# Optimization experiments

Hardware: AMD Instinct MI355X
Metric: run time of the kernel (lower is better)

## Reference

```python
import jax, jax.numpy as jnp
import numpy as np

NUM_GRAPHS = 512


def setup_inputs() -> dict:
    key = jax.random.key(0)
    ks = jax.random.split(key, 8)
    N, E, D, H = 50000, 800000, 128, 128
    x = jax.random.normal(ks[0], (N, D), dtype=jnp.float32)
    edge_attr = jax.random.normal(ks[1], (E, 8), dtype=jnp.float32)
    s = 1.0 / np.sqrt(D)
    W1 = jax.random.normal(ks[2], (D, H), dtype=jnp.float32) * s
    W2 = jax.random.normal(ks[3], (H, H), dtype=jnp.float32) * s
    W3 = jax.random.normal(ks[4], (H, H), dtype=jnp.float32) * s
    b1 = jnp.zeros((H,), jnp.float32)
    b2 = jnp.zeros((H,), jnp.float32)
    b3 = jnp.zeros((H,), jnp.float32)
    edge_index = jax.random.randint(ks[5], (2, E), 0, N, dtype=jnp.int64)
    batch = jnp.sort(jax.random.randint(ks[6], (N,), 0, NUM_GRAPHS, dtype=jnp.int64))
    return {"x": x, "edge_attr": edge_attr, "W1": W1, "b1": b1, "W2": W2,
            "b2": b2, "W3": W3, "b3": b3, "edge_index": edge_index, "batch": batch}


def reference(x, edge_attr, W1, b1, W2, b2, W3, b3, edge_index, batch):
    # edge_attr is accepted but unused (GCNConv ignores it), matching the source.
    N = x.shape[0]
    src, dst = edge_index[0], edge_index[1]
    loop = jnp.arange(N, dtype=src.dtype)
    src_f = jnp.concatenate([src, loop])  # self-loops appended (PyG GCNConv default)
    dst_f = jnp.concatenate([dst, loop])
    # symmetric degree normalization on A + I (deg >= 1 thanks to self-loops)
    deg = jax.ops.segment_sum(jnp.ones(src_f.shape[0], x.dtype), dst_f, num_segments=N)
    dinv = deg ** -0.5
    coef = (dinv[src_f] * dinv[dst_f])[:, None]  # [E+N, 1]

    def gcn_conv(h, W, b):
        h = h @ W                                   # linear first (PyG order)
        agg = jax.ops.segment_sum(h[src_f] * coef, dst_f, num_segments=N)
        return agg + b

    h = jax.nn.relu(gcn_conv(x, W1, b1))   # dropout is identity at inference
    h = jax.nn.relu(gcn_conv(h, W2, b2))
    h = jax.nn.relu(gcn_conv(h, W3, b3))

    # global_mean_pool over graph ids
    sums = jax.ops.segment_sum(h, batch, num_segments=NUM_GRAPHS)
    cnts = jax.ops.segment_sum(jnp.ones((N,), h.dtype), batch, num_segments=NUM_GRAPHS)
    return sums / jnp.maximum(cnts, 1.0)[:, None]
```

## Files before the change

kernel.cpp:

```cpp
#include <hip/hip_runtime.h>
#include <hip/hip_bf16.h>


#define TPB 256
#define CSTRIDE 16
typedef unsigned short u16;
typedef unsigned int u32;
typedef __attribute__((ext_vector_type(8))) __bf16 bf16x8;
typedef __attribute__((ext_vector_type(8))) u16 u16x8;
typedef __attribute__((ext_vector_type(4))) float f32x4;

__device__ __forceinline__ u16 f2b(float f) {
    __bf16 b = (__bf16)f;
    return __builtin_bit_cast(u16, b);
}
__device__ __forceinline__ float b2f_lo(u32 w) { return __builtin_bit_cast(float, w << 16); }
__device__ __forceinline__ float b2f_hi(u32 w) { return __builtin_bit_cast(float, w & 0xffff0000u); }

__device__ __forceinline__ bf16x8 cvt8(float4 u0, float4 u1) {
    u16x8 r;
    r[0] = f2b(u0.x); r[1] = f2b(u0.y); r[2] = f2b(u0.z); r[3] = f2b(u0.w);
    r[4] = f2b(u1.x); r[5] = f2b(u1.y); r[6] = f2b(u1.z); r[7] = f2b(u1.w);
    return __builtin_bit_cast(bf16x8, r);
}

__device__ __forceinline__ void countslot_body(int bid, const int* __restrict__ dst,
                                               int* cnt, u16* __restrict__ aux, int E) {
    int e = (bid * TPB + (int)threadIdx.x) * 4;
    if (e + 3 < E) {
        int4 d = *(const int4*)(dst + e);
        ushort4 a;
        a.x = (u16)atomicAdd(&cnt[d.x * CSTRIDE], 1);
        a.y = (u16)atomicAdd(&cnt[d.y * CSTRIDE], 1);
        a.z = (u16)atomicAdd(&cnt[d.z * CSTRIDE], 1);
        a.w = (u16)atomicAdd(&cnt[d.w * CSTRIDE], 1);
        *(ushort4*)(aux + e) = a;
    } else {
        for (; e < E; ++e) aux[e] = (u16)atomicAdd(&cnt[dst[e] * CSTRIDE], 1);
    }
}

__global__ __launch_bounds__(TPB) void k_scan1(const int* __restrict__ cnt, int* rowptr,
                                               int* bsum, int N) {
    __shared__ int tmp[TPB];
    int t = threadIdx.x;
    int i = blockIdx.x * TPB + t;
    int v = (i < N) ? cnt[(size_t)i * CSTRIDE] : 0;
    tmp[t] = v;
    __syncthreads();
    for (int off = 1; off < TPB; off <<= 1) {
        int y = (t >= off) ? tmp[t - off] : 0;
        __syncthreads();
        tmp[t] += y;
        __syncthreads();
    }
    if (i < N) rowptr[i] = tmp[t] - v;
    if (t == TPB - 1) bsum[blockIdx.x] = tmp[t];
}

__global__ __launch_bounds__(TPB) void k_scan3(int* rowptr, const int* __restrict__ bsum,
                                               const int* __restrict__ cnt, float* dinv,
                                               int N, int total, int nb) {
    __shared__ int tmp[TPB];
    int t = threadIdx.x;
    tmp[t] = (t < nb) ? bsum[t] : 0;
    __syncthreads();
    for (int off = 1; off < TPB; off <<= 1) {
        int y = (t >= off) ? tmp[t - off] : 0;
        __syncthreads();
        tmp[t] += y;
        __syncthreads();
    }
    int pre = (blockIdx.x == 0) ? 0 : tmp[blockIdx.x - 1];
    int i = blockIdx.x * TPB + t;
    if (i < N) {
        rowptr[i] += pre;
        dinv[i] = 1.0f / sqrtf((float)(cnt[(size_t)i * CSTRIDE] + 1));
    }
    if (i == 0) rowptr[N] = total;
}

__global__ __launch_bounds__(TPB) void k_fill_scale(const int* __restrict__ src,
                                                    const int* __restrict__ dst,
                                                    const int* __restrict__ rowptr,
                                                    const u16* __restrict__ aux,
                                                    u16* __restrict__ cols, int E, int nbF,
                                                    u16* __restrict__ g,
                                                    const float* __restrict__ dinv, int N) {
    int b = blockIdx.x;
    if (b < nbF) {
        int e = (b * TPB + (int)threadIdx.x) * 4;
        if (e + 3 < E) {
            int4 s = *(const int4*)(src + e);
            int4 d = *(const int4*)(dst + e);
            ushort4 a = *(const ushort4*)(aux + e);
            cols[rowptr[d.x] + a.x] = (u16)s.x;
            cols[rowptr[d.y] + a.y] = (u16)s.y;
            cols[rowptr[d.z] + a.z] = (u16)s.z;
            cols[rowptr[d.w] + a.w] = (u16)s.w;
        } else {
            for (; e < E; ++e) cols[rowptr[dst[e]] + aux[e]] = (u16)src[e];
        }
    } else {
        int e8 = (b - nbF) * TPB + (int)threadIdx.x;
        if (e8 < N * 16) {
            int row = e8 >> 4;
            int off = (e8 & 15) * 8;
            float dv = dinv[row];
            u16* p = g + (size_t)row * 128 + off;
            uint4 v = *(uint4*)p;
            uint4 o;
            o.x = (u32)f2b(dv * b2f_lo(v.x)) | ((u32)f2b(dv * b2f_hi(v.x)) << 16);
            o.y = (u32)f2b(dv * b2f_lo(v.y)) | ((u32)f2b(dv * b2f_hi(v.y)) << 16);
            o.z = (u32)f2b(dv * b2f_lo(v.z)) | ((u32)f2b(dv * b2f_hi(v.z)) << 16);
            o.w = (u32)f2b(dv * b2f_lo(v.w)) | ((u32)f2b(dv * b2f_hi(v.w)) << 16);
            *(uint4*)p = o;
        }
    }
}

__device__ __forceinline__ void prepw_body(int bb, const float* __restrict__ Wa,
                                           const float* __restrict__ Wb,
                                           const float* __restrict__ Wc,
                                           u16* __restrict__ Wta, u16* __restrict__ Wtb,
                                           u16* __restrict__ Wtc) {
    int m = bb >> 3;
    const float* W = m == 0 ? Wa : (m == 1 ? Wb : Wc);
    u16* Wt = m == 0 ? Wta : (m == 1 ? Wtb : Wtc);
    int t = (bb & 7) * TPB + (int)threadIdx.x;
    int n = t >> 4, c = t & 15;
    u16x8 r;
#pragma unroll
    for (int j = 0; j < 8; ++j) r[j] = f2b(W[(8 * c + j) * 128 + n]);
    int cs = c ^ (n & 15);
    *(u16x8*)(Wt + n * 128 + cs * 8) = r;
}

__global__ __launch_bounds__(TPB) void k_zero_prep(int* cnt, int N, int nbZ4,
                                                   const float* __restrict__ Wa,
                                                   const float* __restrict__ Wb,
                                                   const float* __restrict__ Wc,
                                                   u16* __restrict__ Wta,
                                                   u16* __restrict__ Wtb,
                                                   u16* __restrict__ Wtc,
                                                   u16* __restrict__ bufA,
                                                   u16* __restrict__ bufB) {
    int b = blockIdx.x;
    if (b < nbZ4) {
        int i = b * TPB + (int)threadIdx.x;
        if (i < N * (CSTRIDE / 4)) ((int4*)cnt)[i] = (int4){0, 0, 0, 0};
    } else if (b < nbZ4 + 24) {
        prepw_body(b - nbZ4, Wa, Wb, Wc, Wta, Wtb, Wtc);
    } else {
        int t = threadIdx.x;
        uint4 z = (uint4){0, 0, 0, 0};
        if (t < 16) *(uint4*)(bufA + (size_t)N * 128 + t * 8) = z;
        else if (t < 32) *(uint4*)(bufB + (size_t)N * 128 + (t - 16) * 8) = z;
    }
}

template <bool F32IN, bool SCALE>
__device__ __forceinline__ void gemm_body(int bid, const void* __restrict__ Ain,
                                          const u16* __restrict__ Wt,
                                          u16* __restrict__ C, int N,
                                          const float* __restrict__ dinv) {
    __shared__ u16 Ws[128 * 128];
    int t = threadIdx.x;
    {
        const uint4* s = (const uint4*)Wt;
        uint4* d = (uint4*)Ws;
#pragma unroll
        for (int i = 0; i < 8; ++i) d[t + 256 * i] = s[t + 256 * i];
    }
    __syncthreads();
    int wave = t >> 6, lane = t & 63;
    int li = lane & 15, lq = lane >> 4;
    int r0 = bid * 128 + wave * 32;
    f32x4 acc[2][8];
#pragma unroll
    for (int i = 0; i < 2; ++i)
#pragma unroll
        for (int f = 0; f < 8; ++f) acc[i][f] = (f32x4){0.f, 0.f, 0.f, 0.f};

    int ra = r0 + li, rb = ra + 16;
    size_t ra_c = (size_t)(ra < N ? ra : N - 1);
    size_t rb_c = (size_t)(rb < N ? rb : N - 1);
#pragma unroll
    for (int kc = 0; kc < 4; ++kc) {
        int koff = 32 * kc + 8 * lq;
        bf16x8 a0, a1;
        if constexpr (F32IN) {
            const float* A = (const float*)Ain;
            const float4* p0 = (const float4*)(A + ra_c * 128 + koff);
            const float4* p1 = (const float4*)(A + rb_c * 128 + koff);
            a0 = cvt8(p0[0], p0[1]);
            a1 = cvt8(p1[0], p1[1]);
        } else {
            const u16* A = (const u16*)Ain;
            a0 = *(const bf16x8*)(A + ra_c * 128 + koff);
            a1 = *(const bf16x8*)(A + rb_c * 128 + koff);
        }
#pragma unroll
        for (int f = 0; f < 8; ++f) {
            int n = 16 * f + li;
            int chunk = (4 * kc + lq) ^ li;
            bf16x8 b = *(const bf16x8*)(Ws + n * 128 + chunk * 8);
            acc[0][f] = __builtin_amdgcn_mfma_f32_16x16x32_bf16(a0, b, acc[0][f], 0, 0, 0);
            acc[1][f] = __builtin_amdgcn_mfma_f32_16x16x32_bf16(a1, b, acc[1][f], 0, 0, 0);
        }
    }
#pragma unroll
    for (int ri = 0; ri < 2; ++ri)
#pragma unroll
        for (int r = 0; r < 4; ++r) {
            int row = r0 + 16 * ri + 4 * lq + r;
            if (row < N) {
                float dv = 1.0f;
                if constexpr (SCALE) dv = dinv[row];
#pragma unroll
                for (int f = 0; f < 8; ++f)
                    C[(size_t)row * 128 + 16 * f + li] = f2b(dv * acc[ri][f][r]);
            }
        }
}

template <bool F32IN, bool SCALE>
__global__ __launch_bounds__(TPB) void k_gemm(const void* __restrict__ Ain,
                                              const u16* __restrict__ Wt,
                                              u16* __restrict__ C, int N,
                                              const float* __restrict__ dinv) {
    gemm_body<F32IN, SCALE>(blockIdx.x, Ain, Wt, C, N, dinv);
}

__global__ __launch_bounds__(TPB) void k_gemm1_count(const void* __restrict__ x,
                                                     const u16* __restrict__ Wt1,
                                                     u16* __restrict__ C, int N, int nbG,
                                                     const int* __restrict__ dst,
                                                     int* cnt, u16* __restrict__ aux, int E) {
    int b = blockIdx.x;
    if (b < nbG) {
        gemm_body<true, false>(b, x, Wt1, C, N, nullptr);
    } else {
        countslot_body(b - nbG, dst, cnt, aux, E);
    }
}

#define AGG_ISS(BUF, T)                                                    \
    {                                                                      \
        _Pragma("unroll") for (int u = 0; u < 8; ++u) {                    \
            int col = __shfl(cg[T], u, 8);                                 \
            const u16* p = g + (size_t)col * 128 + fo;                     \
            asm volatile("global_load_dwordx4 %0, %1, off sc0"             \
                         : "=v"(BUF[u]) : "v"(p));                         \
        }                                                                  \
    }
#define AGG_CONS(BUF)                                                      \
    {                                                                      \
        _Pragma("unroll") for (int u = 0; u < 8; ++u) {                    \
            a[0] += b2f_lo(BUF[u].x); a[1] += b2f_hi(BUF[u].x);            \
            a[2] += b2f_lo(BUF[u].y); a[3] += b2f_hi(BUF[u].y);            \
            a[4] += b2f_lo(BUF[u].z); a[5] += b2f_hi(BUF[u].z);            \
            a[6] += b2f_lo(BUF[u].w); a[7] += b2f_hi(BUF[u].w);            \
        }                                                                  \
    }
#define AGG_WAIT(n)                                                        \
    {                                                                      \
        asm volatile("s_waitcnt vmcnt(" #n ")" ::: "memory");              \
        __builtin_amdgcn_sched_barrier(0);                                 \
    }
#define AGG_STEP(T, CUR, NXT)                                              \
    if ((T) < nc) {                                                        \
        if ((T) + 1 < nc) { AGG_ISS(NXT, (T) + 1); AGG_WAIT(8); }          \
        else { AGG_WAIT(0); }                                              \
        AGG_CONS(CUR);                                                     \
    }

__global__ __launch_bounds__(TPB) void k_agg(const u16* __restrict__ g,
                                             const u16* __restrict__ cols,
                                             const int* __restrict__ rowptr,
                                             const float* __restrict__ dinv,
                                             const float* __restrict__ bias,
                                             u16* __restrict__ hout, int N, int hoff) {
    int node = blockIdx.x * 32 + ((int)threadIdx.x >> 3);
    int lane = threadIdx.x & 7;
    if (node >= N) return;
    int fo = hoff + lane * 8;
    int beg = rowptr[node], end = rowptr[node + 1];
    float dn = dinv[node];
    float a[8];
    {
        uint4 vs = *(const uint4*)(g + (size_t)node * 128 + fo);
        a[0] = b2f_lo(vs.x); a[1] = b2f_hi(vs.x);
        a[2] = b2f_lo(vs.y); a[3] = b2f_hi(vs.y);
        a[4] = b2f_lo(vs.z); a[5] = b2f_hi(vs.z);
        a[6] = b2f_lo(vs.w); a[7] = b2f_hi(vs.w);
    }
    for (int sb = beg; sb < end; sb += 64) {
        int m = end - sb;
        if (m > 64) m = 64;
        int cg[8];
#pragma unroll
        for (int q = 0; q < 8; ++q) {
            int off = 8 * q + lane;
            int c = (int)cols[sb + (off < m ? off : 0)];
            cg[q] = (off < m) ? c : N;
        }
        int nc = (m + 7) >> 3;
        uint4 vA[8], vB[8];
        AGG_ISS(vA, 0);
        AGG_STEP(0, vA, vB)
        AGG_STEP(1, vB, vA)
        AGG_STEP(2, vA, vB)
        AGG_STEP(3, vB, vA)
        AGG_STEP(4, vA, vB)
        AGG_STEP(5, vB, vA)
        AGG_STEP(6, vA, vB)
        AGG_STEP(7, vB, vA)
    }
    const float4* bp = (const float4*)(bias + fo);
    float4 b0 = bp[0], b1 = bp[1];
    a[0] = fmaxf(fmaf(dn, a[0], b0.x), 0.f); a[1] = fmaxf(fmaf(dn, a[1], b0.y), 0.f);
    a[2] = fmaxf(fmaf(dn, a[2], b0.z), 0.f); a[3] = fmaxf(fmaf(dn, a[3], b0.w), 0.f);
    a[4] = fmaxf(fmaf(dn, a[4], b1.x), 0.f); a[5] = fmaxf(fmaf(dn, a[5], b1.y), 0.f);
    a[6] = fmaxf(fmaf(dn, a[6], b1.z), 0.f); a[7] = fmaxf(fmaf(dn, a[7], b1.w), 0.f);
    uint4 o;
    o.x = (u32)f2b(a[0]) | ((u32)f2b(a[1]) << 16);
    o.y = (u32)f2b(a[2]) | ((u32)f2b(a[3]) << 16);
    o.z = (u32)f2b(a[4]) | ((u32)f2b(a[5]) << 16);
    o.w = (u32)f2b(a[6]) | ((u32)f2b(a[7]) << 16);
    *(uint4*)(hout + (size_t)node * 128 + fo) = o;
}

__global__ __launch_bounds__(TPB) void k_pool(const u16* __restrict__ h,
                                              const int* __restrict__ batch,
                                              float* __restrict__ out, int N, int G) {
    int g = blockIdx.x;
    int w = threadIdx.x & 63;
    int rid = threadIdx.x >> 6;
    int beg, end;
    {
        int lo = 0, hi = N;
        while (lo < hi) { int m = (lo + hi) >> 1; if (batch[m] < g) lo = m + 1; else hi = m; }
        beg = lo;
        lo = 0; hi = N;
        int g1 = g + 1;
        while (lo < hi) { int m = (lo + hi) >> 1; if (batch[m] < g1) lo = m + 1; else hi = m; }
        end = lo;
    }
    const u32* h32 = (const u32*)h;
    float a0 = 0.f, a1 = 0.f;
#pragma unroll 2
    for (int n = beg + rid; n < end; n += 4) {
        u32 v = h32[(size_t)n * 64 + w];
        a0 += b2f_lo(v); a1 += b2f_hi(v);
    }
    __shared__ float red[4][64][2];
    red[rid][w][0] = a0;
    red[rid][w][1] = a1;
    __syncthreads();
    if (rid == 0) {
        a0 = red[0][w][0] + red[1][w][0] + red[2][w][0] + red[3][w][0];
        a1 = red[0][w][1] + red[1][w][1] + red[2][w][1] + red[3][w][1];
        int c = end - beg; if (c < 1) c = 1;
        float inv = 1.0f / (float)c;
        out[(size_t)g * 128 + 2 * w]     = a0 * inv;
        out[(size_t)g * 128 + 2 * w + 1] = a1 * inv;
    }
}

extern "C" void kernel_launch(void* const* d_in, const int* in_sizes, int n_in,
                              void* d_out, int out_size, void* d_ws, size_t ws_size,
                              hipStream_t stream) {
    const float* x  = (const float*)d_in[0];
    const float* W1 = (const float*)d_in[2];
    const float* b1 = (const float*)d_in[3];
    const float* W2 = (const float*)d_in[4];
    const float* b2 = (const float*)d_in[5];
    const float* W3 = (const float*)d_in[6];
    const float* b3 = (const float*)d_in[7];
    const int* ei    = (const int*)d_in[8];
    const int* batch = (const int*)d_in[9];

    int N = in_sizes[0] / 128;
    int E = in_sizes[8] / 2;
    int G = out_size / 128;
    const int* src = ei;
    const int* dst = ei + E;

    char* w = (char*)d_ws;
    auto alloc = [&](size_t bytes) -> void* {
        void* p = (void*)w;
        w += (bytes + 255) & ~(size_t)255;
        return p;
    };
    int*   cnt    = (int*)alloc((size_t)N * CSTRIDE * 4);
    u16*   aux    = (u16*)alloc((size_t)E * 2);
    int*   rowptr = (int*)alloc((size_t)(N + 1) * 4);
    float* dinv   = (float*)alloc((size_t)N * 4);
    int*   bsum   = (int*)alloc(4096);
    u16*   cols   = (u16*)alloc((size_t)E * 2);
    u16*   Wt1    = (u16*)alloc(128 * 128 * 2);
    u16*   Wt2    = (u16*)alloc(128 * 128 * 2);
    u16*   Wt3    = (u16*)alloc(128 * 128 * 2);
    u16*   bufA   = (u16*)alloc((size_t)(N + 1) * 128 * 2);
    u16*   bufB   = (u16*)alloc((size_t)(N + 1) * 128 * 2);

    int nbN = (N + TPB - 1) / TPB;
    int nbE4 = (E / 4 + TPB - 1) / TPB;
    int nbG = (N + 127) / 128;
    int nbZ4 = (N * (CSTRIDE / 4) + TPB - 1) / TPB;
    int nbS = (N * 16 + TPB - 1) / TPB;
    int nbA = (N + 31) / 32;

    k_zero_prep<<<nbZ4 + 24 + 1, TPB, 0, stream>>>(cnt, N, nbZ4, W1, W2, W3,
                                                   Wt1, Wt2, Wt3, bufA, bufB);
    k_gemm1_count<<<nbG + nbE4, TPB, 0, stream>>>(x, Wt1, bufA, N, nbG, dst, cnt, aux, E);
    k_scan1<<<nbN, TPB, 0, stream>>>(cnt, rowptr, bsum, N);
    k_scan3<<<nbN, TPB, 0, stream>>>(rowptr, bsum, cnt, dinv, N, E, nbN);
    k_fill_scale<<<nbE4 + nbS, TPB, 0, stream>>>(src, dst, rowptr, aux, cols, E, nbE4,
                                                 bufA, dinv, N);

    k_agg<<<nbA, TPB, 0, stream>>>(bufA, cols, rowptr, dinv, b1, bufB, N, 0);
    k_agg<<<nbA, TPB, 0, stream>>>(bufA, cols, rowptr, dinv, b1, bufB, N, 64);
    k_gemm<false, true><<<nbG, TPB, 0, stream>>>(bufB, Wt2, bufA, N, dinv);
    k_agg<<<nbA, TPB, 0, stream>>>(bufA, cols, rowptr, dinv, b2, bufB, N, 0);
    k_agg<<<nbA, TPB, 0, stream>>>(bufA, cols, rowptr, dinv, b2, bufB, N, 64);
    k_gemm<false, true><<<nbG, TPB, 0, stream>>>(bufB, Wt3, bufA, N, dinv);
    k_agg<<<nbA, TPB, 0, stream>>>(bufA, cols, rowptr, dinv, b3, bufB, N, 0);
    k_agg<<<nbA, TPB, 0, stream>>>(bufA, cols, rowptr, dinv, b3, bufB, N, 64);

    k_pool<<<G, TPB, 0, stream>>>(bufB, batch, (float*)d_out, N, G);
}
```

Before: 196.8 us.

## Stage GEMM output through LDS for coalesced stores; cache CSR cols in LDS for aggregation

The GEMM epilogue now writes results into shared memory, then each thread stores full 16-byte rows to global memory, replacing scattered 2-byte stores. The aggregation kernel loads the block's rowptr slice and up to 1024 column indices into shared memory cooperatively, so the per-node gathers read indices from LDS rather than global memory. CSTRIDE is raised from 16 to 32. The changes add barriers and LDS use per block, which may reduce occupancy.

```diff
diff --git a/kernel.cpp b/kernel.cpp
--- a/kernel.cpp
+++ b/kernel.cpp
@@ -3,7 +3,8 @@
 
 
 #define TPB 256
-#define CSTRIDE 16
+#define CSTRIDE 32
+#define COLS_CAP 1024
 typedef unsigned short u16;
 typedef unsigned int u32;
 typedef __attribute__((ext_vector_type(8))) __bf16 bf16x8;
@@ -209,19 +210,30 @@
             acc[1][f] = __builtin_amdgcn_mfma_f32_16x16x32_bf16(a1, b, acc[1][f], 0, 0, 0);
         }
     }
+    __syncthreads();
 #pragma unroll
     for (int ri = 0; ri < 2; ++ri)
 #pragma unroll
         for (int r = 0; r < 4; ++r) {
-            int row = r0 + 16 * ri + 4 * lq + r;
-            if (row < N) {
-                float dv = 1.0f;
-                if constexpr (SCALE) dv = dinv[row];
-#pragma unroll
-                for (int f = 0; f < 8; ++f)
-                    C[(size_t)row * 128 + 16 * f + li] = f2b(dv * acc[ri][f][r]);
+            int rowl = wave * 32 + 16 * ri + 4 * lq + r;
+            float dv = 1.0f;
+            if constexpr (SCALE) {
+                int row = bid * 128 + rowl;
+                dv = (row < N) ? dinv[row] : 1.0f;
             }
-        }
+#pragma unroll
+            for (int f = 0; f < 8; ++f)
+                Ws[rowl * 128 + 16 * f + li] = f2b(dv * acc[ri][f][r]);
+        }
+    __syncthreads();
+#pragma unroll
+    for (int i = 0; i < 8; ++i) {
+        int idx = t + 256 * i;
+        int rowl = idx >> 4, c16 = idx & 15;
+        int row = bid * 128 + rowl;
+        if (row < N)
+            *(uint4*)(C + (size_t)row * 128 + c16 * 8) = ((const uint4*)Ws)[idx];
+    }
 }
 
 template <bool F32IN, bool SCALE>
@@ -281,11 +293,27 @@
                                              const float* __restrict__ dinv,
                                              const float* __restrict__ bias,
                                              u16* __restrict__ hout, int N, int hoff) {
-    int node = blockIdx.x * 32 + ((int)threadIdx.x >> 3);
-    int lane = threadIdx.x & 7;
+    __shared__ u16 sCols[COLS_CAP];
+    __shared__ int sRp[33];
+    int t = threadIdx.x;
+    int node0 = blockIdx.x * 32;
+    if (t < 33) {
+        int idx = node0 + t;
+        if (idx > N) idx = N;
+        sRp[t] = rowptr[idx];
+    }
+    __syncthreads();
+    int blockBeg = sRp[0];
+    int L = sRp[32] - blockBeg;
+    int Lc = L < COLS_CAP ? L : COLS_CAP;
+    for (int i = t; i < Lc; i += TPB) sCols[i] = cols[blockBeg + i];
+    __syncthreads();
+
+    int node = node0 + (t >> 3);
+    int lane = t & 7;
     if (node >= N) return;
     int fo = hoff + lane * 8;
-    int beg = rowptr[node], end = rowptr[node + 1];
+    int beg = sRp[t >> 3], end = sRp[(t >> 3) + 1];
     float dn = dinv[node];
     float a[8];
     {
@@ -302,8 +330,12 @@
 #pragma unroll
         for (int q = 0; q < 8; ++q) {
             int off = 8 * q + lane;
-            int c = (int)cols[sb + (off < m ? off : 0)];
-            cg[q] = (off < m) ? c : N;
+            int gi = sb + (off < m ? off : 0);
+            int lidx = gi - blockBeg;
+            u16 c;
+            if (lidx < COLS_CAP) c = sCols[lidx];
+            else c = cols[gi];
+            cg[q] = (off < m) ? (int)c : N;
         }
         int nc = (m + 7) >> 3;
         uint4 vA[8], vB[8];
```

Measured after the change: 205.6 us. 4.5% more time.
